# Kernel optimization log

Measured on AMD Instinct MI355X. Metric: run time of the kernel, lower is better.

Reference implementation:

```python
import jax, jax.numpy as jnp
import numpy as np

N_NODES = 100000
N_EDGES = 1600000
NFEAT, NHID, NCLASS = 512, 128, 40


def setup_inputs() -> dict:
    key = jax.random.key(0)
    ks = jax.random.split(key, 8)
    features = jax.random.normal(ks[0], (N_NODES, NFEAT), dtype=jnp.float32)
    edge_src = jax.random.randint(ks[1], (N_EDGES,), 0, N_NODES, dtype=jnp.int32)
    edge_dst = jax.random.randint(ks[2], (N_EDGES,), 0, N_NODES, dtype=jnp.int32)
    edge_weight = jax.random.uniform(ks[3], (N_EDGES,), dtype=jnp.float32)
    W1 = jax.random.normal(ks[4], (NFEAT, NHID), dtype=jnp.float32) * (1.0 / np.sqrt(NFEAT))
    b1 = jnp.zeros((NHID,), dtype=jnp.float32)
    W2 = jax.random.normal(ks[5], (NHID, NCLASS), dtype=jnp.float32) * (1.0 / np.sqrt(NHID))
    b2 = jnp.zeros((NCLASS,), dtype=jnp.float32)
    return {"features": features, "edge_src": edge_src, "edge_dst": edge_dst,
            "edge_weight": edge_weight, "W1": W1, "b1": b1, "W2": W2, "b2": b2}


def _gcn_conv(x, W, b, edge_src, edge_dst, edge_weight, num_nodes):
    # GCNconv: adj @ (x @ W) + b, adj given as weighted edge list (spmm).
    h = x @ W                                   # [N, out]
    msgs = edge_weight[:, None] * h[edge_src]   # [E, out] gather + scale
    agg = jax.ops.segment_sum(msgs, edge_dst, num_segments=num_nodes)  # [N, out]
    return agg + b


def reference(features, edge_src, edge_dst, edge_weight, W1, b1, W2, b2):
    x = _gcn_conv(features, W1, b1, edge_src, edge_dst, edge_weight, N_NODES)
    x = jax.nn.relu(x)
    # dropout is identity in eval mode (deterministic reference)
    x = _gcn_conv(x, W2, b2, edge_src, edge_dst, edge_weight, N_NODES)
    return jax.nn.log_softmax(x, axis=1)
```

## Files before the change

### kernel.cpp

```cpp
#include <hip/hip_runtime.h>
#include <hip/hip_bf16.h>
#include <math.h>

#define N_NODES 100000
#define N_EDGES 1600000
#define NFEAT 512
#define NHID 128
#define NCLASS 40

#define BSH 6
#define BNODES (1 << BSH)
#define NBUCK ((N_NODES + BNODES - 1) / BNODES)

#define PCHUNK 4096
#define PEPT 16
#define PNB ((N_EDGES + PCHUNK - 1) / PCHUNK)

#define PCHUNK2 8192
#define FPNB ((N_EDGES + PCHUNK2 - 1) / PCHUNK2)
#define GEMM1_NB ((N_NODES + 127) / 128)

#define CAP 1536
#define KSTG 6

typedef short bf16x8 __attribute__((ext_vector_type(8)));
typedef float f32x4 __attribute__((ext_vector_type(4)));

static __device__ __forceinline__ unsigned short f32_to_bf16(float f) {
    unsigned int u = __float_as_uint(f);
    unsigned int r = u + 0x7FFFu + ((u >> 16) & 1u);
    return (unsigned short)(r >> 16);
}
static __device__ __forceinline__ float bf16_to_f32(unsigned short h) {
    return __uint_as_float(((unsigned int)h) << 16);
}

__global__ __launch_bounds__(256) void bucket_hist_transpose_kernel(
    const int* __restrict__ dst, int* __restrict__ histG,
    const float* __restrict__ W1, unsigned short* __restrict__ Wt,
    const float* __restrict__ W2, unsigned short* __restrict__ W2t, int E)
{
    const int blk = blockIdx.x;
    if (blk >= PNB + 256) {
        int i = (blk - PNB - 256) * 256 + threadIdx.x;
        if (i < 48 * 128) {
            int c = i >> 7;
            int k = i & 127;
            W2t[i] = (c < NCLASS) ? f32_to_bf16(W2[k * NCLASS + c]) : 0;
        }
        return;
    }
    if (blk >= PNB) {
        int tid2 = (blk - PNB) * 256 + threadIdx.x;
        int n = tid2 >> 9;
        int k = tid2 & 511;
        Wt[tid2] = f32_to_bf16(W1[k * NHID + n]);
        return;
    }
    __shared__ int hl[NBUCK];
    const int t = threadIdx.x;
    for (int j = t; j < NBUCK; j += 256) hl[j] = 0;
    __syncthreads();
    const int c0 = blk * PCHUNK;
    #pragma unroll
    for (int i = 0; i < PEPT; i++) {
        int e = c0 + t + i * 256;
        if (e < E) atomicAdd(&hl[dst[e] >> BSH], 1);
    }
    __syncthreads();
    for (int j = t; j < NBUCK; j += 256) {
        int c = hl[j];
        if (c) atomicAdd(&histG[j * 16], c);
    }
}

__global__ __launch_bounds__(1024) void bucket_scan_kernel(
    const int* __restrict__ histG, int* __restrict__ bofs,
    int* __restrict__ bcursor)
{
    __shared__ int sh[1024];
    const int t = threadIdx.x;
    const int i0 = 2 * t, i1 = 2 * t + 1;
    int v0 = (i0 < NBUCK) ? histG[i0 * 16] : 0;
    int v1 = (i1 < NBUCK) ? histG[i1 * 16] : 0;
    int s = v0 + v1;
    sh[t] = s;
    __syncthreads();
    #pragma unroll
    for (int off = 1; off < 1024; off <<= 1) {
        int u = (t >= off) ? sh[t - off] : 0;
        __syncthreads();
        sh[t] += u;
        __syncthreads();
    }
    int base = sh[t] - s;
    if (i0 < NBUCK) { bofs[i0] = base;      bcursor[i0] = base; }
    if (i1 < NBUCK) { bofs[i1] = base + v0; bcursor[i1] = base + v0; }
    if (t == 1023) bofs[NBUCK] = sh[1023];
}

__global__ __launch_bounds__(256) void partition_gemm1_kernel(
    const int* __restrict__ src, const int* __restrict__ dstp,
    const float* __restrict__ w, int* __restrict__ bcursor,
    int2* __restrict__ sortedA,
    const float* __restrict__ A, const unsigned short* __restrict__ Wt,
    unsigned short* __restrict__ h1b, int E, int M)
{
    __shared__ __align__(16) char smem[4 * 32 * 130 * 2];

    const int tid = threadIdx.x;

    if (blockIdx.x < FPNB) {
        int* hist  = (int*)smem;
        int* bbase = hist + NBUCK;
        const int c0 = blockIdx.x * PCHUNK2;

        for (int j = tid; j < NBUCK; j += 256) hist[j] = 0;
        __syncthreads();

        #pragma unroll
        for (int i = 0; i < PCHUNK2 / 256; i++) {
            int e = c0 + tid + i * 256;
            if (e < E) atomicAdd(&hist[dstp[e] >> BSH], 1);
        }
        __syncthreads();

        for (int j = tid; j < NBUCK; j += 256) {
            int c = hist[j];
            bbase[j] = c ? atomicAdd(&bcursor[j], c) : 0;
        }
        __syncthreads();

        #pragma unroll
        for (int i = 0; i < PCHUNK2 / 256; i++) {
            int e = c0 + tid + i * 256;
            if (e < E) {
                int d = dstp[e];
                int p = atomicAdd(&bbase[d >> BSH], 1);
                sortedA[p] = make_int2(src[e] | ((d & (BNODES - 1)) << 17),
                                       __float_as_int(w[e]));
            }
        }
        return;
    }

    unsigned short (*cstage)[32 * 130] = (unsigned short (*)[32 * 130])smem;

    const int w4 = tid >> 6;
    const int lane = tid & 63;
    const int lr = lane & 15;
    const int quad = lane >> 4;
    const int m0 = (blockIdx.x - FPNB) * 128 + w4 * 32;

    f32x4 acc[2][8];
    #pragma unroll
    for (int rt = 0; rt < 2; rt++)
        #pragma unroll
        for (int ct = 0; ct < 8; ct++)
            acc[rt][ct] = (f32x4){0.f, 0.f, 0.f, 0.f};

    int r0 = m0 + lr;
    int r1 = m0 + 16 + lr;
    int r0c = r0 < M ? r0 : M - 1;
    int r1c = r1 < M ? r1 : M - 1;
    const float* a0p = A + (size_t)r0c * NFEAT + quad * 8;
    const float* a1p = A + (size_t)r1c * NFEAT + quad * 8;
    const unsigned short* bp = Wt + (size_t)lr * NFEAT + quad * 8;

    #pragma unroll 2
    for (int k0 = 0; k0 < NFEAT; k0 += 32) {
        float4 a0a = *(const float4*)(a0p + k0);
        float4 a0b = *(const float4*)(a0p + k0 + 4);
        float4 a1a = *(const float4*)(a1p + k0);
        float4 a1b = *(const float4*)(a1p + k0 + 4);

        bf16x8 fb[8];
        #pragma unroll
        for (int ct = 0; ct < 8; ct++)
            fb[ct] = *(const bf16x8*)(bp + (size_t)ct * 16 * NFEAT + k0);

        bf16x8 fa0, fa1;
        fa0[0] = (short)f32_to_bf16(a0a.x); fa0[1] = (short)f32_to_bf16(a0a.y);
        fa0[2] = (short)f32_to_bf16(a0a.z); fa0[3] = (short)f32_to_bf16(a0a.w);
        fa0[4] = (short)f32_to_bf16(a0b.x); fa0[5] = (short)f32_to_bf16(a0b.y);
        fa0[6] = (short)f32_to_bf16(a0b.z); fa0[7] = (short)f32_to_bf16(a0b.w);
        fa1[0] = (short)f32_to_bf16(a1a.x); fa1[1] = (short)f32_to_bf16(a1a.y);
        fa1[2] = (short)f32_to_bf16(a1a.z); fa1[3] = (short)f32_to_bf16(a1a.w);
        fa1[4] = (short)f32_to_bf16(a1b.x); fa1[5] = (short)f32_to_bf16(a1b.y);
        fa1[6] = (short)f32_to_bf16(a1b.z); fa1[7] = (short)f32_to_bf16(a1b.w);

        #pragma unroll
        for (int ct = 0; ct < 8; ct++) {
            acc[0][ct] = __builtin_amdgcn_mfma_f32_16x16x32_bf16(fa0, fb[ct], acc[0][ct], 0, 0, 0);
            acc[1][ct] = __builtin_amdgcn_mfma_f32_16x16x32_bf16(fa1, fb[ct], acc[1][ct], 0, 0, 0);
        }
    }

    unsigned short* st = cstage[w4];
    #pragma unroll
    for (int rt = 0; rt < 2; rt++)
        #pragma unroll
        for (int ct = 0; ct < 8; ct++)
            #pragma unroll
            for (int i = 0; i < 4; i++) {
                int row = rt * 16 + quad * 4 + i;
                int col = ct * 16 + lr;
                st[row * 130 + col] = f32_to_bf16(acc[rt][ct][i]);
            }

    #pragma unroll
    for (int g = 0; g < 8; g++) {
        int row = g * 4 + (lane >> 4);
        int c8 = lane & 15;
        const unsigned short* rp = &st[row * 130 + c8 * 8];
        uint4 v = *(const uint4*)rp;
        int gr = m0 + row;
        if (gr < M)
            *(uint4*)&h1b[(size_t)gr * NHID + c8 * 8] = v;
    }
}

__global__ __launch_bounds__(256) void agg1_gemm2_kernel(
    const int2* __restrict__ sortedA, const int* __restrict__ bofs,
    const unsigned short* __restrict__ h1b, const float* __restrict__ b1,
    const unsigned short* __restrict__ W2t, float* __restrict__ h2, int N)
{
    __shared__ __align__(16) int2 ebuf[CAP];
    __shared__ __align__(16) unsigned short xs[64][136];
    __shared__ __align__(16) unsigned short wt2s[48 * 136];
    __shared__ int ncnt[BNODES];
    __shared__ int nofs[BNODES];
    __shared__ int ncur[BNODES];
    __shared__ int sc[BNODES];
    __shared__ float b1s[128];

    const int tid = threadIdx.x;
    const int b = blockIdx.x;
    const int node0 = b << BSH;
    const int nn = min(BNODES, N - node0);
    const int beg = bofs[b];
    const int end = bofs[b + 1];
    const int cnt = end - beg;
    const bool fits = (cnt <= CAP);

    for (int i = tid; i < 48 * 128; i += 256)
        wt2s[(i >> 7) * 136 + (i & 127)] = W2t[i];
    if (tid < 128) b1s[tid] = b1[tid];
    if (tid < BNODES) ncnt[tid] = 0;
    __syncthreads();

    int2 myrec[KSTG];
    if (fits) {
        #pragma unroll
        for (int k = 0; k < KSTG; k++) {
            int i = tid + k * 256;
            if (i < cnt) {
                int2 r = sortedA[beg + i];
                myrec[k] = r;
                atomicAdd(&ncnt[(r.x >> 17) & (BNODES - 1)], 1);
            }
        }
        __syncthreads();
        if (tid < BNODES) sc[tid] = ncnt[tid];
        __syncthreads();
        #pragma unroll
        for (int off = 1; off < BNODES; off <<= 1) {
            int u = (tid < BNODES && tid >= off) ? sc[tid - off] : 0;
            __syncthreads();
            if (tid < BNODES) sc[tid] += u;
            __syncthreads();
        }
        if (tid < BNODES) {
            int e0 = sc[tid] - ncnt[tid];
            nofs[tid] = e0;
            ncur[tid] = e0;
        }
        __syncthreads();
        #pragma unroll
        for (int k = 0; k < KSTG; k++) {
            int i = tid + k * 256;
            if (i < cnt) {
                int nd = (myrec[k].x >> 17) & (BNODES - 1);
                int p = atomicAdd(&ncur[nd], 1);
                ebuf[p] = myrec[k];
            }
        }
        __syncthreads();
    }

    const int g = tid >> 5;
    const int lane = tid & 31;
    const unsigned short* hb = h1b + lane * 4;

    for (int ln = g * 8; ln < g * 8 + 8; ln++) {
        if (ln >= nn) break;
        float4 acc = {0.f, 0.f, 0.f, 0.f};
        if (fits) {
            const int s0 = nofs[ln];
            const int c0 = ncnt[ln];
            int j = 0;
            for (; j + 8 <= c0; j += 8) {
                int2 r[8];
                #pragma unroll
                for (int q = 0; q < 8; q++) r[q] = ebuf[s0 + j + q];
                ushort4 hv[8];
                #pragma unroll
                for (int q = 0; q < 8; q++)
                    hv[q] = *(const ushort4*)(hb + (size_t)(r[q].x & 0x1FFFF) * NHID);
                #pragma unroll
                for (int q = 0; q < 8; q++) {
                    float wj = __int_as_float(r[q].y);
                    acc.x = fmaf(wj, bf16_to_f32(hv[q].x), acc.x);
                    acc.y = fmaf(wj, bf16_to_f32(hv[q].y), acc.y);
                    acc.z = fmaf(wj, bf16_to_f32(hv[q].z), acc.z);
                    acc.w = fmaf(wj, bf16_to_f32(hv[q].w), acc.w);
                }
            }
            for (; j + 4 <= c0; j += 4) {
                int2 r[4];
                #pragma unroll
                for (int q = 0; q < 4; q++) r[q] = ebuf[s0 + j + q];
                ushort4 hv[4];
                #pragma unroll
                for (int q = 0; q < 4; q++)
                    hv[q] = *(const ushort4*)(hb + (size_t)(r[q].x & 0x1FFFF) * NHID);
                #pragma unroll
                for (int q = 0; q < 4; q++) {
                    float wj = __int_as_float(r[q].y);
                    acc.x = fmaf(wj, bf16_to_f32(hv[q].x), acc.x);
                    acc.y = fmaf(wj, bf16_to_f32(hv[q].y), acc.y);
                    acc.z = fmaf(wj, bf16_to_f32(hv[q].z), acc.z);
                    acc.w = fmaf(wj, bf16_to_f32(hv[q].w), acc.w);
                }
            }
            for (; j < c0; j++) {
                int2 r = ebuf[s0 + j];
                float wj = __int_as_float(r.y);
                ushort4 hv = *(const ushort4*)(hb + (size_t)(r.x & 0x1FFFF) * NHID);
                acc.x = fmaf(wj, bf16_to_f32(hv.x), acc.x);
                acc.y = fmaf(wj, bf16_to_f32(hv.y), acc.y);
                acc.z = fmaf(wj, bf16_to_f32(hv.z), acc.z);
                acc.w = fmaf(wj, bf16_to_f32(hv.w), acc.w);
            }
        } else {
            for (int e = beg; e < end; e++) {
                int2 r = sortedA[e];
                if (((r.x >> 17) & (BNODES - 1)) == ln) {
                    float wj = __int_as_float(r.y);
                    ushort4 hv = *(const ushort4*)(hb + (size_t)(r.x & 0x1FFFF) * NHID);
                    acc.x = fmaf(wj, bf16_to_f32(hv.x), acc.x);
                    acc.y = fmaf(wj, bf16_to_f32(hv.y), acc.y);
                    acc.z = fmaf(wj, bf16_to_f32(hv.z), acc.z);
                    acc.w = fmaf(wj, bf16_to_f32(hv.w), acc.w);
                }
            }
        }
        float4 bb = *(const float4*)&b1s[lane * 4];
        ushort4 px;
        px.x = f32_to_bf16(fmaxf(acc.x + bb.x, 0.f));
        px.y = f32_to_bf16(fmaxf(acc.y + bb.y, 0.f));
        px.z = f32_to_bf16(fmaxf(acc.z + bb.z, 0.f));
        px.w = f32_to_bf16(fmaxf(acc.w + bb.w, 0.f));
        *(ushort4*)&xs[ln][lane * 4] = px;
    }
    __syncthreads();

    const int wv = tid >> 6;
    const int l64 = tid & 63;
    const int lr = l64 & 15;
    const int quad = l64 >> 4;

    f32x4 c_[3];
    #pragma unroll
    for (int nt = 0; nt < 3; nt++)
        c_[nt] = (f32x4){0.f, 0.f, 0.f, 0.f};

    #pragma unroll
    for (int k0 = 0; k0 < 128; k0 += 32) {
        bf16x8 af = *(const bf16x8*)&xs[wv * 16 + lr][k0 + quad * 8];
        bf16x8 bf_[3];
        #pragma unroll
        for (int nt = 0; nt < 3; nt++)
            bf_[nt] = *(const bf16x8*)&wt2s[(nt * 16 + lr) * 136 + k0 + quad * 8];
        #pragma unroll
        for (int nt = 0; nt < 3; nt++)
            c_[nt] = __builtin_amdgcn_mfma_f32_16x16x32_bf16(
                af, bf_[nt], c_[nt], 0, 0, 0);
    }

    #pragma unroll
    for (int nt = 0; nt < 3; nt++) {
        int col = nt * 16 + lr;
        if (col < NCLASS) {
            #pragma unroll
            for (int i = 0; i < 4; i++) {
                int row = wv * 16 + quad * 4 + i;
                if (row < nn)
                    h2[(size_t)(node0 + row) * NCLASS + col] = c_[nt][i];
            }
        }
    }
}

__global__ __launch_bounds__(256) void agg2_softmax_kernel(
    const int2* __restrict__ sortedA, const int* __restrict__ bofs,
    const float* __restrict__ h2, const float* __restrict__ b2,
    float* __restrict__ out, int N)
{
    __shared__ __align__(16) int2 ebuf[CAP];
    __shared__ int ncnt[BNODES];
    __shared__ int nofs[BNODES];
    __shared__ int ncur[BNODES];
    __shared__ int sc[BNODES];

    const int tid = threadIdx.x;
    const int b = blockIdx.x;
    const int node0 = b << BSH;
    const int nn = min(BNODES, N - node0);
    const int beg = bofs[b];
    const int end = bofs[b + 1];
    const int cnt = end - beg;
    const bool fits = (cnt <= CAP);

    if (tid < BNODES) ncnt[tid] = 0;
    __syncthreads();

    int2 myrec[KSTG];
    if (fits) {
        #pragma unroll
        for (int k = 0; k < KSTG; k++) {
            int i = tid + k * 256;
            if (i < cnt) {
                int2 r = sortedA[beg + i];
                myrec[k] = r;
                atomicAdd(&ncnt[(r.x >> 17) & (BNODES - 1)], 1);
            }
        }
        __syncthreads();
        if (tid < BNODES) sc[tid] = ncnt[tid];
        __syncthreads();
        #pragma unroll
        for (int off = 1; off < BNODES; off <<= 1) {
            int u = (tid < BNODES && tid >= off) ? sc[tid - off] : 0;
            __syncthreads();
            if (tid < BNODES) sc[tid] += u;
            __syncthreads();
        }
        if (tid < BNODES) {
            int e0 = sc[tid] - ncnt[tid];
            nofs[tid] = e0;
            ncur[tid] = e0;
        }
        __syncthreads();
        #pragma unroll
        for (int k = 0; k < KSTG; k++) {
            int i = tid + k * 256;
            if (i < cnt) {
                int nd = (myrec[k].x >> 17) & (BNODES - 1);
                int p = atomicAdd(&ncur[nd], 1);
                ebuf[p] = myrec[k];
            }
        }
        __syncthreads();
    }

    const int grp = tid >> 4;
    const int l16 = tid & 15;
    const float* hp0 = h2 + l16 * 4;

    for (int it = 0; it < 4; it++) {
        const int ln = it * 16 + grp;
        float4 acc = {0.f, 0.f, 0.f, 0.f};
        if (ln < nn) {
            if (fits) {
                const int s0 = nofs[ln];
                const int c0 = ncnt[ln];
                int j = 0;
                for (; j + 8 <= c0; j += 8) {
                    int2 r[8];
                    #pragma unroll
                    for (int q = 0; q < 8; q++) r[q] = ebuf[s0 + j + q];
                    if (l16 < 10) {
                        float4 v[8];
                        #pragma unroll
                        for (int q = 0; q < 8; q++)
                            v[q] = *(const float4*)(hp0 + (size_t)(r[q].x & 0x1FFFF) * NCLASS);
                        #pragma unroll
                        for (int q = 0; q < 8; q++) {
                            float wj = __int_as_float(r[q].y);
                            acc.x = fmaf(wj, v[q].x, acc.x);
                            acc.y = fmaf(wj, v[q].y, acc.y);
                            acc.z = fmaf(wj, v[q].z, acc.z);
                            acc.w = fmaf(wj, v[q].w, acc.w);
                        }
                    }
                }
                for (; j + 4 <= c0; j += 4) {
                    int2 r[4];
                    #pragma unroll
                    for (int q = 0; q < 4; q++) r[q] = ebuf[s0 + j + q];
                    if (l16 < 10) {
                        float4 v[4];
                        #pragma unroll
                        for (int q = 0; q < 4; q++)
                            v[q] = *(const float4*)(hp0 + (size_t)(r[q].x & 0x1FFFF) * NCLASS);
                        #pragma unroll
                        for (int q = 0; q < 4; q++) {
                            float wj = __int_as_float(r[q].y);
                            acc.x = fmaf(wj, v[q].x, acc.x);
                            acc.y = fmaf(wj, v[q].y, acc.y);
                            acc.z = fmaf(wj, v[q].z, acc.z);
                            acc.w = fmaf(wj, v[q].w, acc.w);
                        }
                    }
                }
                for (; j < c0; j++) {
                    int2 r = ebuf[s0 + j];
                    if (l16 < 10) {
                        float wj = __int_as_float(r.y);
                        float4 v = *(const float4*)(hp0 + (size_t)(r.x & 0x1FFFF) * NCLASS);
                        acc.x = fmaf(wj, v.x, acc.x);
                        acc.y = fmaf(wj, v.y, acc.y);
                        acc.z = fmaf(wj, v.z, acc.z);
                        acc.w = fmaf(wj, v.w, acc.w);
                    }
                }
            } else {
                for (int e = beg; e < end; e++) {
                    int2 r = sortedA[e];
                    if (((r.x >> 17) & (BNODES - 1)) == ln && l16 < 10) {
                        float wj = __int_as_float(r.y);
                        float4 v = *(const float4*)(hp0 + (size_t)(r.x & 0x1FFFF) * NCLASS);
                        acc.x = fmaf(wj, v.x, acc.x);
                        acc.y = fmaf(wj, v.y, acc.y);
                        acc.z = fmaf(wj, v.z, acc.z);
                        acc.w = fmaf(wj, v.w, acc.w);
                    }
                }
            }
        }
        bool act = (ln < nn) && (l16 < 10);
        float mx = -INFINITY;
        if (act) {
            float4 bb = *(const float4*)&b2[l16 * 4];
            acc.x += bb.x; acc.y += bb.y; acc.z += bb.z; acc.w += bb.w;
            mx = fmaxf(fmaxf(acc.x, acc.y), fmaxf(acc.z, acc.w));
        }
        #pragma unroll
        for (int o = 8; o > 0; o >>= 1) mx = fmaxf(mx, __shfl_xor(mx, o, 16));
        float sm = act ? expf(acc.x - mx) + expf(acc.y - mx) +
                         expf(acc.z - mx) + expf(acc.w - mx) : 0.f;
        #pragma unroll
        for (int o = 8; o > 0; o >>= 1) sm += __shfl_xor(sm, o, 16);
        if (act) {
            float l = mx + logf(sm);
            float4 o4 = {acc.x - l, acc.y - l, acc.z - l, acc.w - l};
            *(float4*)&out[(size_t)(node0 + ln) * NCLASS + l16 * 4] = o4;
        }
    }
}

extern "C" void kernel_launch(void* const* d_in, const int* in_sizes, int n_in,
                              void* d_out, int out_size, void* d_ws, size_t ws_size,
                              hipStream_t stream) {
    const float* features = (const float*)d_in[0];
    const int* edge_src   = (const int*)d_in[1];
    const int* edge_dst   = (const int*)d_in[2];
    const float* edge_w   = (const float*)d_in[3];
    const float* W1       = (const float*)d_in[4];
    const float* b1       = (const float*)d_in[5];
    const float* W2       = (const float*)d_in[6];
    const float* b2       = (const float*)d_in[7];
    float* out = (float*)d_out;

    char* base = (char*)d_ws;
    float*          h2       = (float*)base;
    unsigned short* h1b      = (unsigned short*)(base + 51200000);
    unsigned short* Wt       = (unsigned short*)(base + 76800000);
    int*            histG    = (int*)(base + 76931072);
    int*            bofs     = (int*)(base + 77040000);
    int*            bcursor  = (int*)(base + 77050000);
    unsigned short* W2t      = (unsigned short*)(base + 77060000);
    int2*           sortedA  = (int2*)(base + 90540000);

    hipMemsetAsync(histG, 0, NBUCK * 16 * sizeof(int), stream);

    bucket_hist_transpose_kernel<<<PNB + 256 + 24, 256, 0, stream>>>(
        edge_dst, histG, W1, Wt, W2, W2t, N_EDGES);
    bucket_scan_kernel<<<1, 1024, 0, stream>>>(histG, bofs, bcursor);

    partition_gemm1_kernel<<<FPNB + GEMM1_NB, 256, 0, stream>>>(
        edge_src, edge_dst, edge_w, bcursor, sortedA,
        features, Wt, h1b, N_EDGES, N_NODES);

    agg1_gemm2_kernel<<<NBUCK, 256, 0, stream>>>(
        sortedA, bofs, h1b, b1, W2t, h2, N_NODES);

    agg2_softmax_kernel<<<NBUCK, 256, 0, stream>>>(
        sortedA, bofs, h2, b2, out, N_NODES);
}
```

Before: 533.7 us.

## Split partition from GEMM1 and stage partitioned edges in LDS for coalesced writes

Separates the fused edge-partition/GEMM1 kernel into two kernels. The partition now does a block-local counting sort in shared memory (per-bucket local scan plus global bucket reservation), then writes edges out contiguously instead of scattering each edge directly. This aims to reduce scattered global writes, at the cost of an extra launch, large shared memory use per block and losing overlap between partition and GEMM1.

```diff
diff --git a/kernel.cpp b/kernel.cpp
--- a/kernel.cpp
+++ b/kernel.cpp
@@ -15,10 +15,6 @@
 #define PCHUNK 4096
 #define PEPT 16
 #define PNB ((N_EDGES + PCHUNK - 1) / PCHUNK)
-
-#define PCHUNK2 8192
-#define FPNB ((N_EDGES + PCHUNK2 - 1) / PCHUNK2)
-#define GEMM1_NB ((N_NODES + 127) / 128)
 
 #define CAP 1536
 #define KSTG 6
@@ -99,58 +95,100 @@
     if (t == 1023) bofs[NBUCK] = sh[1023];
 }
 
-__global__ __launch_bounds__(256) void partition_gemm1_kernel(
+__global__ __launch_bounds__(256) void partition_kernel(
     const int* __restrict__ src, const int* __restrict__ dstp,
     const float* __restrict__ w, int* __restrict__ bcursor,
-    int2* __restrict__ sortedA,
-    const float* __restrict__ A, const unsigned short* __restrict__ Wt,
-    unsigned short* __restrict__ h1b, int E, int M)
+    int2* __restrict__ sortedA, int E)
 {
-    __shared__ __align__(16) char smem[4 * 32 * 130 * 2];
+    __shared__ int lcur[NBUCK];
+    __shared__ int lofs[NBUCK];
+    __shared__ int gbase[NBUCK];
+    __shared__ int psum[256];
+    __shared__ __align__(16) int2 ebuf[PCHUNK];
+    __shared__ int gpos[PCHUNK];
+
+    const int t = threadIdx.x;
+    const int c0 = blockIdx.x * PCHUNK;
+    const int cnt = min(PCHUNK, E - c0);
+
+    for (int j = t; j < NBUCK; j += 256) lcur[j] = 0;
+    __syncthreads();
+
+    int  myb[PEPT];
+    int2 myv[PEPT];
+    #pragma unroll
+    for (int i = 0; i < PEPT; i++) {
+        int e = c0 + t + i * 256;
+        if (e < E) {
+            int d = dstp[e];
+            myb[i] = d >> BSH;
+            myv[i] = make_int2(src[e] | ((d & (BNODES - 1)) << 17),
+                               __float_as_int(w[e]));
+            atomicAdd(&lcur[myb[i]], 1);
+        } else {
+            myb[i] = -1;
+        }
+    }
+    __syncthreads();
+
+    int c[7];
+    int s = 0;
+    #pragma unroll
+    for (int k = 0; k < 7; k++) {
+        int j = t * 7 + k;
+        c[k] = (j < NBUCK) ? lcur[j] : 0;
+        s += c[k];
+    }
+    psum[t] = s;
+    __syncthreads();
+    #pragma unroll
+    for (int off = 1; off < 256; off <<= 1) {
+        int u = (t >= off) ? psum[t - off] : 0;
+        __syncthreads();
+        psum[t] += u;
+        __syncthreads();
+    }
+    int run = psum[t] - s;
+    #pragma unroll
+    for (int k = 0; k < 7; k++) {
+        int j = t * 7 + k;
+        if (j < NBUCK) {
+            lofs[j] = run;
+            lcur[j] = run;
+            gbase[j] = c[k] ? atomicAdd(&bcursor[j], c[k]) : 0;
+            run += c[k];
+        }
+    }
+    __syncthreads();
+
+    #pragma unroll
+    for (int i = 0; i < PEPT; i++) {
+        if (myb[i] >= 0) {
+            int p = atomicAdd(&lcur[myb[i]], 1);
+            ebuf[p] = myv[i];
+            gpos[p] = gbase[myb[i]] + (p - lofs[myb[i]]);
+        }
+    }
+    __syncthreads();
+
+    for (int i = t; i < cnt; i += 256)
+        sortedA[gpos[i]] = ebuf[i];
+}
+
+__global__ __launch_bounds__(256) void gemm1_mfma_kernel(
+    const float* __restrict__ A,
+    const unsigned short* __restrict__ Wt,
+    unsigned short* __restrict__ h1b,
+    int M)
+{
+    __shared__ unsigned short cstage[4][32 * 130];
 
     const int tid = threadIdx.x;
-
-    if (blockIdx.x < FPNB) {
-        int* hist  = (int*)smem;
-        int* bbase = hist + NBUCK;
-        const int c0 = blockIdx.x * PCHUNK2;
-
-        for (int j = tid; j < NBUCK; j += 256) hist[j] = 0;
-        __syncthreads();
-
-        #pragma unroll
-        for (int i = 0; i < PCHUNK2 / 256; i++) {
-            int e = c0 + tid + i * 256;
-            if (e < E) atomicAdd(&hist[dstp[e] >> BSH], 1);
-        }
-        __syncthreads();
-
-        for (int j = tid; j < NBUCK; j += 256) {
-            int c = hist[j];
-            bbase[j] = c ? atomicAdd(&bcursor[j], c) : 0;
-        }
-        __syncthreads();
-
-        #pragma unroll
-        for (int i = 0; i < PCHUNK2 / 256; i++) {
-            int e = c0 + tid + i * 256;
-            if (e < E) {
-                int d = dstp[e];
-                int p = atomicAdd(&bbase[d >> BSH], 1);
-                sortedA[p] = make_int2(src[e] | ((d & (BNODES - 1)) << 17),
-                                       __float_as_int(w[e]));
-            }
-        }
-        return;
-    }
-
-    unsigned short (*cstage)[32 * 130] = (unsigned short (*)[32 * 130])smem;
-
     const int w4 = tid >> 6;
     const int lane = tid & 63;
     const int lr = lane & 15;
     const int quad = lane >> 4;
-    const int m0 = (blockIdx.x - FPNB) * 128 + w4 * 32;
+    const int m0 = blockIdx.x * 128 + w4 * 32;
 
     f32x4 acc[2][8];
     #pragma unroll
@@ -589,9 +627,11 @@
         edge_dst, histG, W1, Wt, W2, W2t, N_EDGES);
     bucket_scan_kernel<<<1, 1024, 0, stream>>>(histG, bofs, bcursor);
 
-    partition_gemm1_kernel<<<FPNB + GEMM1_NB, 256, 0, stream>>>(
-        edge_src, edge_dst, edge_w, bcursor, sortedA,
-        features, Wt, h1b, N_EDGES, N_NODES);
+    partition_kernel<<<PNB, 256, 0, stream>>>(
+        edge_src, edge_dst, edge_w, bcursor, sortedA, N_EDGES);
+
+    gemm1_mfma_kernel<<<(N_NODES + 127) / 128, 256, 0, stream>>>(
+        features, Wt, h1b, N_NODES);
 
     agg1_gemm2_kernel<<<NBUCK, 256, 0, stream>>>(
         sortedA, bofs, h1b, b1, W2t, h2, N_NODES);
```

New measurement: 586.0 us. 1.1x slower.
